# Optimization experiments

Hardware: AMD Instinct MI355X
Metric: run time of the kernel (lower is better)

Reference implementation:

```python
import jax, jax.numpy as jnp
import numpy as np

MARGIN = 0.2
EPS = 1e-8


def setup_inputs() -> dict:
    key = jax.random.key(0)
    k1, k2, k3 = jax.random.split(key, 3)
    B, D, T, C = 4096, 512, 65536, 100
    batch = jax.random.normal(k1, (B, D), dtype=jnp.float32)
    beta = jnp.ones((C,), dtype=jnp.float32) * 1.2  # learned per-class beta param
    labels = jax.random.randint(k2, (B,), 0, C)
    triplets = jax.random.randint(k3, (T, 3), 0, B)
    return {"batch": batch, "beta": beta, "labels": labels, "triplets": triplets}


def reference(batch, beta, labels, triplets):
    # Gather anchor / positive / negative embeddings: [T, D]
    a = batch[triplets[:, 0]]
    p = batch[triplets[:, 1]]
    n = batch[triplets[:, 2]]
    d_ap = jnp.sqrt(jnp.sum((a - p) ** 2, axis=-1) + EPS)  # [T]
    d_an = jnp.sqrt(jnp.sum((a - n) ** 2, axis=-1) + EPS)  # [T]
    b = beta[labels[triplets[:, 0]]]  # per-anchor-class beta, [T]
    pos_loss = jax.nn.relu(d_ap - b + MARGIN)
    neg_loss = jax.nn.relu(b - d_an + MARGIN)
    # torch bool+bool is logical OR; count triplets with any active hinge
    pair_count = jnp.sum(((pos_loss > 0.0) | (neg_loss > 0.0)).astype(jnp.float32))
    total = jnp.sum(pos_loss + neg_loss)
    loss = jnp.where(pair_count > 0.0, total / jnp.maximum(pair_count, 1.0), total)
    return loss
```

## Files before the change

### kernel.cpp

```cpp
#include <hip/hip_runtime.h>

#define MARGIN 0.2f
#define EPS_    1e-8f
#define BM 128
#define BK 64

typedef __attribute__((ext_vector_type(8))) short short8;
typedef __attribute__((ext_vector_type(4))) float f32x4;

__device__ __forceinline__ unsigned pack_bf16(float lo, float hi)
{
    union { float f; unsigned u; } a, b;
    a.f = lo; b.f = hi;
    unsigned ua = (a.u + 0x7fffu + ((a.u >> 16) & 1u)) >> 16;
    unsigned ub = (b.u + 0x7fffu + ((b.u >> 16) & 1u)) & 0xffff0000u;
    return ua | ub;
}

__device__ __forceinline__ unsigned short bf16_1(float x)
{
    union { float f; unsigned u; } v;
    v.f = x;
    return (unsigned short)((v.u + 0x7fffu + ((v.u >> 16) & 1u)) >> 16);
}

__global__ __launch_bounds__(256) void prep_kernel(
    const float* __restrict__ in, uint4* __restrict__ out, int n8,
    float* __restrict__ norms, int B,
    float* __restrict__ ws_total, unsigned int* __restrict__ ws_cnt,
    unsigned int* __restrict__ ws_done)
{
    const int i = blockIdx.x * blockDim.x + threadIdx.x;
    if (i == 0) { *ws_total = 0.0f; *ws_cnt = 0u; *ws_done = 0u; }
    float s = 0.0f;
    if (i < n8) {
        const float4 a = ((const float4*)in)[2 * i + 0];
        const float4 b = ((const float4*)in)[2 * i + 1];
        uint4 r;
        r.x = pack_bf16(a.x, a.y);
        r.y = pack_bf16(a.z, a.w);
        r.z = pack_bf16(b.x, b.y);
        r.w = pack_bf16(b.z, b.w);
        out[i] = r;
        s = a.x * a.x + a.y * a.y + a.z * a.z + a.w * a.w
          + b.x * b.x + b.y * b.y + b.z * b.z + b.w * b.w;
    }
    #pragma unroll
    for (int off = 1; off < 64; off <<= 1)
        s += __shfl_xor(s, off, 64);
    const int row = i >> 6;
    if ((threadIdx.x & 63) == 0 && row < B) norms[row] = s;
}

__global__ __launch_bounds__(256) void gemm_xxt(
    const char* __restrict__ xb,
    unsigned short* __restrict__ G, int B, int D, int NB)
{
    int lin = blockIdx.x, bm = 0, rowlen = NB;
    while (lin >= rowlen) { lin -= rowlen; ++bm; --rowlen; }
    const int bn = bm + lin;

    __shared__ char At[2][BM * BK * 2];
    __shared__ char Bt[2][BM * BK * 2];
    const int tid  = threadIdx.x;
    const int lane = tid & 63;
    const int w    = tid >> 6;
    const int wr   = w >> 1, wc = w & 1;
    const int rowb = D * 2;

    f32x4 acc[4][4] = {};

    const int ssw = (((lane & 7) * 16) ^ ((lane >> 3) << 4));

    auto stage = [&](int kk, int p) {
        #pragma unroll
        for (int c4 = 0; c4 < 4; ++c4) {
            const int c = w * 4 + c4;
            const size_t arow = (size_t)bm * BM + c * 8 + (lane >> 3);
            const size_t brow = (size_t)bn * BM + c * 8 + (lane >> 3);
            const char* asrc = xb + arow * rowb + kk * (BK * 2) + ssw;
            const char* bsrc = xb + brow * rowb + kk * (BK * 2) + ssw;
            __builtin_amdgcn_global_load_lds((const unsigned*)asrc,
                (unsigned*)(At[p] + c * 1024 + lane * 16), 16, 0, 0);
            __builtin_amdgcn_global_load_lds((const unsigned*)bsrc,
                (unsigned*)(Bt[p] + c * 1024 + lane * 16), 16, 0, 0);
        }
    };

    const int rsw = (lane & 7) << 4;
    const int nk = D / BK;
    stage(0, 0);
    for (int kk = 0; kk < nk; ++kk) {
        const int p = kk & 1;
        if (kk + 1 < nk) {
            stage(kk + 1, p ^ 1);
            asm volatile("s_waitcnt vmcnt(8)" ::: "memory");
        } else {
            asm volatile("s_waitcnt vmcnt(0)" ::: "memory");
        }
        __builtin_amdgcn_s_barrier();
        __builtin_amdgcn_sched_barrier(0);

        #pragma unroll
        for (int ks = 0; ks < 2; ++ks) {
            const int kbyte = (ks * 64 + (lane >> 4) * 16) ^ rsw;
            short8 a[4], b[4];
            #pragma unroll
            for (int m = 0; m < 4; ++m) {
                const int row = wr * 64 + m * 16 + (lane & 15);
                a[m] = *(const short8*)(At[p] + row * 128 + kbyte);
            }
            #pragma unroll
            for (int n = 0; n < 4; ++n) {
                const int row = wc * 64 + n * 16 + (lane & 15);
                b[n] = *(const short8*)(Bt[p] + row * 128 + kbyte);
            }
            #pragma unroll
            for (int m = 0; m < 4; ++m)
                #pragma unroll
                for (int n = 0; n < 4; ++n)
                    acc[m][n] = __builtin_amdgcn_mfma_f32_16x16x32_bf16(
                        a[m], b[n], acc[m][n], 0, 0, 0);
        }
        asm volatile("s_waitcnt lgkmcnt(0)" ::: "memory");
        __builtin_amdgcn_sched_barrier(0);
        __builtin_amdgcn_s_barrier();
    }

    #pragma unroll
    for (int m = 0; m < 4; ++m)
        #pragma unroll
        for (int n = 0; n < 4; ++n)
            #pragma unroll
            for (int j = 0; j < 4; ++j) {
                const int row = bm * BM + wr * 64 + m * 16 + (lane >> 4) * 4 + j;
                const int col = bn * BM + wc * 64 + n * 16 + (lane & 15);
                G[(size_t)row * B + col] = bf16_1(acc[m][n][j]);
            }
}

__global__ __launch_bounds__(256) void tri_eval(
    const unsigned short* __restrict__ G,
    const float* __restrict__ norms,
    const float* __restrict__ beta,
    const int*   __restrict__ labels,
    const int*   __restrict__ trip,
    int B, int T,
    float*        __restrict__ ws_total,
    unsigned int* __restrict__ ws_cnt,
    unsigned int* __restrict__ ws_done,
    float*        __restrict__ out)
{
    const int i = blockIdx.x * blockDim.x + threadIdx.x;
    float pn = 0.0f;
    int   c  = 0;
    if (i < T) {
        const int t0 = trip[3 * i + 0];
        const int t1 = trip[3 * i + 1];
        const int t2 = trip[3 * i + 2];
        const int r1 = t0 < t1 ? t0 : t1, c1 = t0 < t1 ? t1 : t0;
        const int r2 = t0 < t2 ? t0 : t2, c2 = t0 < t2 ? t2 : t0;
        union { unsigned u; float f; } v1, v2;
        v1.u = (unsigned)G[(size_t)r1 * B + c1] << 16;
        v2.u = (unsigned)G[(size_t)r2 * B + c2] << 16;
        const float n0  = norms[t0];
        const float n1  = norms[t1];
        const float n2  = norms[t2];
        const float b   = beta[labels[t0]];
        const float dap = sqrtf(fmaxf(n0 + n1 - 2.0f * v1.f, 0.0f) + EPS_);
        const float dan = sqrtf(fmaxf(n0 + n2 - 2.0f * v2.f, 0.0f) + EPS_);
        const float pos = fmaxf(dap - b + MARGIN, 0.0f);
        const float neg = fmaxf(b - dan + MARGIN, 0.0f);
        pn = pos + neg;
        c  = ((pos > 0.0f) || (neg > 0.0f)) ? 1 : 0;
    }
    #pragma unroll
    for (int off = 1; off < 64; off <<= 1) {
        pn += __shfl_xor(pn, off, 64);
        c  += __shfl_xor(c,  off, 64);
    }
    __shared__ float s_tot[4];
    __shared__ int   s_cnt[4];
    const int wid = threadIdx.x >> 6;
    if ((threadIdx.x & 63) == 0) { s_tot[wid] = pn; s_cnt[wid] = c; }
    __syncthreads();
    if (threadIdx.x == 0) {
        atomicAdd(ws_total, s_tot[0] + s_tot[1] + s_tot[2] + s_tot[3]);
        atomicAdd(ws_cnt, (unsigned)(s_cnt[0] + s_cnt[1] + s_cnt[2] + s_cnt[3]));
        __threadfence();
        const unsigned done = atomicAdd(ws_done, 1u);
        if (done == gridDim.x - 1) {
            const float    total = atomicAdd(ws_total, 0.0f);
            const unsigned pcnt  = atomicAdd(ws_cnt, 0u);
            const float pc = (float)pcnt;
            out[0] = (pc > 0.0f) ? (total / fmaxf(pc, 1.0f)) : total;
        }
    }
}

__global__ __launch_bounds__(256) void triplet_loss_generic(
    const float* __restrict__ batch,
    const float* __restrict__ beta,
    const int*   __restrict__ labels,
    const int*   __restrict__ triplets,
    int T, int D,
    float*        __restrict__ ws_total,
    unsigned int* __restrict__ ws_cnt)
{
    const int lane   = threadIdx.x & 63;
    const int wid    = threadIdx.x >> 6;
    const int gwave  = (blockIdx.x * blockDim.x + threadIdx.x) >> 6;
    const int nwaves = (gridDim.x * blockDim.x) >> 6;
    const int dq     = D >> 2;

    float        tot = 0.0f;
    unsigned int cnt = 0u;

    for (int t = gwave; t < T; t += nwaves) {
        const int t0 = triplets[3 * t + 0];
        const int t1 = triplets[3 * t + 1];
        const int t2 = triplets[3 * t + 2];
        const float4* A = (const float4*)(batch + (size_t)t0 * D);
        const float4* P = (const float4*)(batch + (size_t)t1 * D);
        const float4* N = (const float4*)(batch + (size_t)t2 * D);
        float sap = 0.0f, san = 0.0f;
        for (int idx = lane; idx < dq; idx += 64) {
            const float4 av = A[idx];
            const float4 pv = P[idx];
            const float4 nv = N[idx];
            float dx = av.x - pv.x, dy = av.y - pv.y, dz = av.z - pv.z, dw = av.w - pv.w;
            sap += dx * dx + dy * dy + dz * dz + dw * dw;
            dx = av.x - nv.x; dy = av.y - nv.y; dz = av.z - nv.z; dw = av.w - nv.w;
            san += dx * dx + dy * dy + dz * dz + dw * dw;
        }
        #pragma unroll
        for (int off = 1; off < 64; off <<= 1) {
            sap += __shfl_xor(sap, off, 64);
            san += __shfl_xor(san, off, 64);
        }
        if (lane == 0) {
            const float d_ap = sqrtf(sap + EPS_);
            const float d_an = sqrtf(san + EPS_);
            const float b    = beta[labels[t0]];
            const float pos  = fmaxf(d_ap - b + MARGIN, 0.0f);
            const float neg  = fmaxf(b - d_an + MARGIN, 0.0f);
            tot += pos + neg;
            cnt += ((pos > 0.0f) || (neg > 0.0f)) ? 1u : 0u;
        }
    }

    __shared__ float        s_tot[4];
    __shared__ unsigned int s_cnt[4];
    if (lane == 0) { s_tot[wid] = tot; s_cnt[wid] = cnt; }
    __syncthreads();
    if (threadIdx.x == 0) {
        float        bt = 0.0f;
        unsigned int bc = 0u;
        const int nw = blockDim.x >> 6;
        for (int i = 0; i < nw; ++i) { bt += s_tot[i]; bc += s_cnt[i]; }
        atomicAdd(ws_total, bt);
        atomicAdd(ws_cnt, bc);
    }
}

__global__ void finalize_kernel(const float* __restrict__ ws_total,
                                const unsigned int* __restrict__ ws_cnt,
                                float* __restrict__ out)
{
    const float total = ws_total[0];
    const float pc    = (float)ws_cnt[0];
    out[0] = (pc > 0.0f) ? (total / fmaxf(pc, 1.0f)) : total;
}

extern "C" void kernel_launch(void* const* d_in, const int* in_sizes, int n_in,
                              void* d_out, int out_size, void* d_ws, size_t ws_size,
                              hipStream_t stream)
{
    const float* batch    = (const float*)d_in[0];
    const float* beta     = (const float*)d_in[1];
    const int*   labels   = (const int*)d_in[2];
    const int*   triplets = (const int*)d_in[3];

    const int B = in_sizes[2];
    const int D = in_sizes[0] / B;
    const int T = in_sizes[3] / 3;

    float*        ws_total = (float*)d_ws;
    unsigned int* ws_cnt   = (unsigned int*)((char*)d_ws + 4);
    unsigned int* ws_done  = (unsigned int*)((char*)d_ws + 8);

    const size_t nm_off = 4096;
    const size_t hb_off = 32768;
    const size_t g_off  = (hb_off + (size_t)B * D * 2 + 255) & ~(size_t)255;
    const size_t need   = g_off + (size_t)B * B * 2;

    const bool fast = (B % BM == 0) && (D == 512) && (ws_size >= need) &&
                      (T >= 1) && (nm_off + (size_t)B * 4 <= hb_off);

    if (fast) {
        float*          norms = (float*)((char*)d_ws + nm_off);
        uint4*          hb    = (uint4*)((char*)d_ws + hb_off);
        unsigned short* G     = (unsigned short*)((char*)d_ws + g_off);

        const int n8 = (B * D) / 8;
        prep_kernel<<<(n8 + 255) / 256, 256, 0, stream>>>(
            batch, hb, n8, norms, B, ws_total, ws_cnt, ws_done);

        const int NB = B / BM;
        const int nblk = NB * (NB + 1) / 2;
        gemm_xxt<<<nblk, 256, 0, stream>>>((const char*)hb, G, B, D, NB);

        tri_eval<<<(T + 255) / 256, 256, 0, stream>>>(
            G, norms, beta, labels, triplets, B, T,
            ws_total, ws_cnt, ws_done, (float*)d_out);
    } else {
        (void)hipMemsetAsync(d_ws, 0, 12, stream);
        const int block = 256;
        int grid = 2048;
        const int max_grid = (T + 3) / 4;
        if (grid > max_grid) grid = max_grid;
        triplet_loss_generic<<<grid, block, 0, stream>>>(
            batch, beta, labels, triplets, T, D, ws_total, ws_cnt);
        finalize_kernel<<<1, 1, 0, stream>>>(ws_total, ws_cnt, (float*)d_out);
    }
}
```

Baseline: 45.90 us.

## Fuse bf16 conversion and norm computation into Gram GEMM, drop prep kernel

Removes the separate prep kernel. The GEMM now stages fp32 rows straight into LDS and converts them to bf16 in registers with v_cvt_pk_bf16_f32. Squared norms are read from the diagonal of the Gram accumulators, and the tile index is remapped so consecutive tiles land on the same XCD. This saves one launch and the bf16 intermediate round trip, but doubles the global and LDS bytes per K step, and the norms now carry bf16 input precision instead of fp32.

```diff
diff --git a/kernel.cpp b/kernel.cpp
--- a/kernel.cpp
+++ b/kernel.cpp
@@ -3,19 +3,10 @@
 #define MARGIN 0.2f
 #define EPS_    1e-8f
 #define BM 128
-#define BK 64
+#define BKF 32
 
 typedef __attribute__((ext_vector_type(8))) short short8;
 typedef __attribute__((ext_vector_type(4))) float f32x4;
-
-__device__ __forceinline__ unsigned pack_bf16(float lo, float hi)
-{
-    union { float f; unsigned u; } a, b;
-    a.f = lo; b.f = hi;
-    unsigned ua = (a.u + 0x7fffu + ((a.u >> 16) & 1u)) >> 16;
-    unsigned ub = (b.u + 0x7fffu + ((b.u >> 16) & 1u)) & 0xffff0000u;
-    return ua | ub;
-}
 
 __device__ __forceinline__ unsigned short bf16_1(float x)
 {
@@ -24,49 +15,48 @@
     return (unsigned short)((v.u + 0x7fffu + ((v.u >> 16) & 1u)) >> 16);
 }
 
-__global__ __launch_bounds__(256) void prep_kernel(
-    const float* __restrict__ in, uint4* __restrict__ out, int n8,
-    float* __restrict__ norms, int B,
+__device__ __forceinline__ short8 frag_f32(const char* base, int row, int hi)
+{
+    const int sw = (row & 7) << 4;
+    const f32x4 lo = *(const f32x4*)(base + row * 128 + ((hi * 32) ^ sw));
+    const f32x4 hh = *(const f32x4*)(base + row * 128 + ((hi * 32 + 16) ^ sw));
+    union { short8 s; unsigned u[4]; } r;
+    asm("v_cvt_pk_bf16_f32 %0, %1, %2" : "=v"(r.u[0]) : "v"(lo[0]), "v"(lo[1]));
+    asm("v_cvt_pk_bf16_f32 %0, %1, %2" : "=v"(r.u[1]) : "v"(lo[2]), "v"(lo[3]));
+    asm("v_cvt_pk_bf16_f32 %0, %1, %2" : "=v"(r.u[2]) : "v"(hh[0]), "v"(hh[1]));
+    asm("v_cvt_pk_bf16_f32 %0, %1, %2" : "=v"(r.u[3]) : "v"(hh[2]), "v"(hh[3]));
+    return r.s;
+}
+
+__global__ __launch_bounds__(256) void gemm_fused(
+    const float* __restrict__ xf,
+    unsigned short* __restrict__ G,
+    float* __restrict__ norms,
+    int B, int D, int NB, int ntiles,
     float* __restrict__ ws_total, unsigned int* __restrict__ ws_cnt,
     unsigned int* __restrict__ ws_done)
 {
-    const int i = blockIdx.x * blockDim.x + threadIdx.x;
-    if (i == 0) { *ws_total = 0.0f; *ws_cnt = 0u; *ws_done = 0u; }
-    float s = 0.0f;
-    if (i < n8) {
-        const float4 a = ((const float4*)in)[2 * i + 0];
-        const float4 b = ((const float4*)in)[2 * i + 1];
-        uint4 r;
-        r.x = pack_bf16(a.x, a.y);
-        r.y = pack_bf16(a.z, a.w);
-        r.z = pack_bf16(b.x, b.y);
-        r.w = pack_bf16(b.z, b.w);
-        out[i] = r;
-        s = a.x * a.x + a.y * a.y + a.z * a.z + a.w * a.w
-          + b.x * b.x + b.y * b.y + b.z * b.z + b.w * b.w;
-    }
-    #pragma unroll
-    for (int off = 1; off < 64; off <<= 1)
-        s += __shfl_xor(s, off, 64);
-    const int row = i >> 6;
-    if ((threadIdx.x & 63) == 0 && row < B) norms[row] = s;
-}
-
-__global__ __launch_bounds__(256) void gemm_xxt(
-    const char* __restrict__ xb,
-    unsigned short* __restrict__ G, int B, int D, int NB)
-{
-    int lin = blockIdx.x, bm = 0, rowlen = NB;
+    if (blockIdx.x == 0 && threadIdx.x == 0) {
+        *ws_total = 0.0f; *ws_cnt = 0u; *ws_done = 0u;
+    }
+
+    const int q = ntiles >> 3, r8 = ntiles & 7;
+    const int xcd = blockIdx.x & 7, idx = blockIdx.x >> 3;
+    int lin = ((xcd < r8) ? xcd * (q + 1) : r8 * (q + 1) + (xcd - r8) * q) + idx;
+
+    int bm = 0, rowlen = NB;
     while (lin >= rowlen) { lin -= rowlen; ++bm; --rowlen; }
     const int bn = bm + lin;
 
-    __shared__ char At[2][BM * BK * 2];
-    __shared__ char Bt[2][BM * BK * 2];
+    __shared__ char At[2][BM * BKF * 4];
+    __shared__ char Bt[2][BM * BKF * 4];
     const int tid  = threadIdx.x;
     const int lane = tid & 63;
     const int w    = tid >> 6;
     const int wr   = w >> 1, wc = w & 1;
-    const int rowb = D * 2;
+    const int rowb = D * 4;
+    const int l15  = lane & 15;
+    const int hi   = lane >> 4;
 
     f32x4 acc[4][4] = {};
 
@@ -78,8 +68,8 @@
             const int c = w * 4 + c4;
             const size_t arow = (size_t)bm * BM + c * 8 + (lane >> 3);
             const size_t brow = (size_t)bn * BM + c * 8 + (lane >> 3);
-            const char* asrc = xb + arow * rowb + kk * (BK * 2) + ssw;
-            const char* bsrc = xb + brow * rowb + kk * (BK * 2) + ssw;
+            const char* asrc = (const char*)xf + arow * rowb + kk * (BKF * 4) + ssw;
+            const char* bsrc = (const char*)xf + brow * rowb + kk * (BKF * 4) + ssw;
             __builtin_amdgcn_global_load_lds((const unsigned*)asrc,
                 (unsigned*)(At[p] + c * 1024 + lane * 16), 16, 0, 0);
             __builtin_amdgcn_global_load_lds((const unsigned*)bsrc,
@@ -87,8 +77,7 @@
         }
     };
 
-    const int rsw = (lane & 7) << 4;
-    const int nk = D / BK;
+    const int nk = D / BKF;
     stage(0, 0);
     for (int kk = 0; kk < nk; ++kk) {
         const int p = kk & 1;
@@ -101,40 +90,39 @@
         __builtin_amdgcn_s_barrier();
         __builtin_amdgcn_sched_barrier(0);
 
-        #pragma unroll
-        for (int ks = 0; ks < 2; ++ks) {
-            const int kbyte = (ks * 64 + (lane >> 4) * 16) ^ rsw;
-            short8 a[4], b[4];
+        short8 a[4], b[4];
+        #pragma unroll
+        for (int m = 0; m < 4; ++m)
+            a[m] = frag_f32(At[p], wr * 64 + m * 16 + l15, hi);
+        #pragma unroll
+        for (int n = 0; n < 4; ++n)
+            b[n] = frag_f32(Bt[p], wc * 64 + n * 16 + l15, hi);
+        #pragma unroll
+        for (int m = 0; m < 4; ++m)
             #pragma unroll
-            for (int m = 0; m < 4; ++m) {
-                const int row = wr * 64 + m * 16 + (lane & 15);
-                a[m] = *(const short8*)(At[p] + row * 128 + kbyte);
-            }
-            #pragma unroll
-            for (int n = 0; n < 4; ++n) {
-                const int row = wc * 64 + n * 16 + (lane & 15);
-                b[n] = *(const short8*)(Bt[p] + row * 128 + kbyte);
-            }
-            #pragma unroll
-            for (int m = 0; m < 4; ++m)
-                #pragma unroll
-                for (int n = 0; n < 4; ++n)
-                    acc[m][n] = __builtin_amdgcn_mfma_f32_16x16x32_bf16(
-                        a[m], b[n], acc[m][n], 0, 0, 0);
-        }
+            for (int n = 0; n < 4; ++n)
+                acc[m][n] = __builtin_amdgcn_mfma_f32_16x16x32_bf16(
+                    a[m], b[n], acc[m][n], 0, 0, 0);
+
         asm volatile("s_waitcnt lgkmcnt(0)" ::: "memory");
         __builtin_amdgcn_sched_barrier(0);
         __builtin_amdgcn_s_barrier();
     }
 
+    if (bm == bn && wr == wc && (l15 >> 2) == hi) {
+        #pragma unroll
+        for (int m = 0; m < 4; ++m)
+            norms[bm * BM + wr * 64 + m * 16 + l15] = acc[m][m][l15 & 3];
+    }
+
     #pragma unroll
     for (int m = 0; m < 4; ++m)
         #pragma unroll
         for (int n = 0; n < 4; ++n)
             #pragma unroll
             for (int j = 0; j < 4; ++j) {
-                const int row = bm * BM + wr * 64 + m * 16 + (lane >> 4) * 4 + j;
-                const int col = bn * BM + wc * 64 + n * 16 + (lane & 15);
+                const int row = bm * BM + wr * 64 + m * 16 + hi * 4 + j;
+                const int col = bn * BM + wc * 64 + n * 16 + l15;
                 G[(size_t)row * B + col] = bf16_1(acc[m][n][j]);
             }
 }
@@ -290,25 +278,20 @@
     unsigned int* ws_done  = (unsigned int*)((char*)d_ws + 8);
 
     const size_t nm_off = 4096;
-    const size_t hb_off = 32768;
-    const size_t g_off  = (hb_off + (size_t)B * D * 2 + 255) & ~(size_t)255;
+    const size_t g_off  = 32768;
     const size_t need   = g_off + (size_t)B * B * 2;
 
-    const bool fast = (B % BM == 0) && (D == 512) && (ws_size >= need) &&
-                      (T >= 1) && (nm_off + (size_t)B * 4 <= hb_off);
+    const bool fast = (B % BM == 0) && (D % BKF == 0) && (ws_size >= need) &&
+                      (T >= 1) && (nm_off + (size_t)B * 4 <= g_off);
 
     if (fast) {
         float*          norms = (float*)((char*)d_ws + nm_off);
-        uint4*          hb    = (uint4*)((char*)d_ws + hb_off);
         unsigned short* G     = (unsigned short*)((char*)d_ws + g_off);
 
-        const int n8 = (B * D) / 8;
-        prep_kernel<<<(n8 + 255) / 256, 256, 0, stream>>>(
-            batch, hb, n8, norms, B, ws_total, ws_cnt, ws_done);
-
         const int NB = B / BM;
-        const int nblk = NB * (NB + 1) / 2;
-        gemm_xxt<<<nblk, 256, 0, stream>>>((const char*)hb, G, B, D, NB);
+        const int ntiles = NB * (NB + 1) / 2;
+        gemm_fused<<<ntiles, 256, 0, stream>>>(
+            batch, G, norms, B, D, NB, ntiles, ws_total, ws_cnt, ws_done);
 
         tri_eval<<<(T + 255) / 256, 256, 0, stream>>>(
             G, norms, beta, labels, triplets, B, T,
```

Result: slower. 53.85 us (+17.3%).

## Halve GEMM K-tile and remap tiles to XCDs for L2 locality

Applied to the files above, without the earlier changes.

Cuts the K-tile of the triangular X·Xᵀ GEMM from 64 to 32, which halves LDS use per block and changes the staging layout, swizzle and wait counts to match. It also remaps block indices so that each of the 8 XCDs gets a contiguous range of upper-triangle tiles, so neighbouring tiles that reuse the same rows share an L2. The smaller K step aims for higher occupancy but doubles the number of barriers per K and leaves fewer MFMAs between each sync.

```diff
diff --git a/kernel.cpp b/kernel.cpp
--- a/kernel.cpp
+++ b/kernel.cpp
@@ -3,7 +3,7 @@
 #define MARGIN 0.2f
 #define EPS_    1e-8f
 #define BM 128
-#define BK 64
+#define BK 32
 
 typedef __attribute__((ext_vector_type(8))) short short8;
 typedef __attribute__((ext_vector_type(4))) float f32x4;
@@ -54,9 +54,13 @@
 
 __global__ __launch_bounds__(256) void gemm_xxt(
     const char* __restrict__ xb,
-    unsigned short* __restrict__ G, int B, int D, int NB)
-{
-    int lin = blockIdx.x, bm = 0, rowlen = NB;
+    unsigned short* __restrict__ G, int B, int D, int NB, int ntiles)
+{
+    const int q = ntiles >> 3, r8 = ntiles & 7;
+    const int xcd = blockIdx.x & 7, idx = blockIdx.x >> 3;
+    int lin = ((xcd < r8) ? xcd * (q + 1) : r8 * (q + 1) + (xcd - r8) * q) + idx;
+
+    int bm = 0, rowlen = NB;
     while (lin >= rowlen) { lin -= rowlen; ++bm; --rowlen; }
     const int bn = bm + lin;
 
@@ -67,17 +71,20 @@
     const int w    = tid >> 6;
     const int wr   = w >> 1, wc = w & 1;
     const int rowb = D * 2;
+    const int l15  = lane & 15;
+    const int hi   = lane >> 4;
 
     f32x4 acc[4][4] = {};
 
-    const int ssw = (((lane & 7) * 16) ^ ((lane >> 3) << 4));
+    const int lrow = lane >> 2;
+    const int ssw  = ((lane & 3) * 16) ^ ((lrow & 3) << 4);
 
     auto stage = [&](int kk, int p) {
         #pragma unroll
-        for (int c4 = 0; c4 < 4; ++c4) {
-            const int c = w * 4 + c4;
-            const size_t arow = (size_t)bm * BM + c * 8 + (lane >> 3);
-            const size_t brow = (size_t)bn * BM + c * 8 + (lane >> 3);
+        for (int c2 = 0; c2 < 2; ++c2) {
+            const int c = w * 2 + c2;
+            const size_t arow = (size_t)bm * BM + c * 16 + lrow;
+            const size_t brow = (size_t)bn * BM + c * 16 + lrow;
             const char* asrc = xb + arow * rowb + kk * (BK * 2) + ssw;
             const char* bsrc = xb + brow * rowb + kk * (BK * 2) + ssw;
             __builtin_amdgcn_global_load_lds((const unsigned*)asrc,
@@ -87,41 +94,39 @@
         }
     };
 
-    const int rsw = (lane & 7) << 4;
+    const int rsw = (l15 & 3) << 4;
     const int nk = D / BK;
     stage(0, 0);
     for (int kk = 0; kk < nk; ++kk) {
         const int p = kk & 1;
         if (kk + 1 < nk) {
             stage(kk + 1, p ^ 1);
-            asm volatile("s_waitcnt vmcnt(8)" ::: "memory");
+            asm volatile("s_waitcnt vmcnt(4)" ::: "memory");
         } else {
             asm volatile("s_waitcnt vmcnt(0)" ::: "memory");
         }
         __builtin_amdgcn_s_barrier();
         __builtin_amdgcn_sched_barrier(0);
 
-        #pragma unroll
-        for (int ks = 0; ks < 2; ++ks) {
-            const int kbyte = (ks * 64 + (lane >> 4) * 16) ^ rsw;
-            short8 a[4], b[4];
+        const int kbyte = (hi * 16) ^ rsw;
+        short8 a[4], b[4];
+        #pragma unroll
+        for (int m = 0; m < 4; ++m) {
+            const int row = wr * 64 + m * 16 + l15;
+            a[m] = *(const short8*)(At[p] + row * 64 + kbyte);
+        }
+        #pragma unroll
+        for (int n = 0; n < 4; ++n) {
+            const int row = wc * 64 + n * 16 + l15;
+            b[n] = *(const short8*)(Bt[p] + row * 64 + kbyte);
+        }
+        #pragma unroll
+        for (int m = 0; m < 4; ++m)
             #pragma unroll
-            for (int m = 0; m < 4; ++m) {
-                const int row = wr * 64 + m * 16 + (lane & 15);
-                a[m] = *(const short8*)(At[p] + row * 128 + kbyte);
-            }
-            #pragma unroll
-            for (int n = 0; n < 4; ++n) {
-                const int row = wc * 64 + n * 16 + (lane & 15);
-                b[n] = *(const short8*)(Bt[p] + row * 128 + kbyte);
-            }
-            #pragma unroll
-            for (int m = 0; m < 4; ++m)
-                #pragma unroll
-                for (int n = 0; n < 4; ++n)
-                    acc[m][n] = __builtin_amdgcn_mfma_f32_16x16x32_bf16(
-                        a[m], b[n], acc[m][n], 0, 0, 0);
-        }
+            for (int n = 0; n < 4; ++n)
+                acc[m][n] = __builtin_amdgcn_mfma_f32_16x16x32_bf16(
+                    a[m], b[n], acc[m][n], 0, 0, 0);
+
         asm volatile("s_waitcnt lgkmcnt(0)" ::: "memory");
         __builtin_amdgcn_sched_barrier(0);
         __builtin_amdgcn_s_barrier();
@@ -133,8 +138,8 @@
         for (int n = 0; n < 4; ++n)
             #pragma unroll
             for (int j = 0; j < 4; ++j) {
-                const int row = bm * BM + wr * 64 + m * 16 + (lane >> 4) * 4 + j;
-                const int col = bn * BM + wc * 64 + n * 16 + (lane & 15);
+                const int row = bm * BM + wr * 64 + m * 16 + hi * 4 + j;
+                const int col = bn * BM + wc * 64 + n * 16 + l15;
                 G[(size_t)row * B + col] = bf16_1(acc[m][n][j]);
             }
 }
@@ -307,8 +312,9 @@
             batch, hb, n8, norms, B, ws_total, ws_cnt, ws_done);
 
         const int NB = B / BM;
-        const int nblk = NB * (NB + 1) / 2;
-        gemm_xxt<<<nblk, 256, 0, stream>>>((const char*)hb, G, B, D, NB);
+        const int ntiles = NB * (NB + 1) / 2;
+        gemm_xxt<<<ntiles, 256, 0, stream>>>(
+            (const char*)hb, G, B, D, NB, ntiles);
 
         tri_eval<<<(T + 255) / 256, 256, 0, stream>>>(
             G, norms, beta, labels, triplets, B, T,
```

After: 42.89 us (median of 2 runs). -6.6%, faster.
